# Kernel tuning notes

Hardware: AMD Instinct MI355X
Metric: run time of the kernel (lower is better)

## Reference

```python
import jax, jax.numpy as jnp
import numpy as np

D_MODEL = 1024
N_HEAD = 16
HEAD_DIM = D_MODEL // N_HEAD


def setup_inputs() -> dict:
    key = jax.random.key(0)
    k1, k2, k3 = jax.random.split(key, 3)
    B, T = 2, 2048
    x = jax.random.normal(k1, (B, T, D_MODEL), dtype=jnp.float32)
    # nn.MultiheadAttention packed in-projection: (3*D, D), xavier-like scale
    w_in = jax.random.normal(k2, (3 * D_MODEL, D_MODEL), dtype=jnp.float32) * (1.0 / np.sqrt(D_MODEL))
    b_in = jnp.zeros((3 * D_MODEL,), dtype=jnp.float32)
    w_out = jax.random.normal(k3, (D_MODEL, D_MODEL), dtype=jnp.float32) * (1.0 / np.sqrt(D_MODEL))
    b_out = jnp.zeros((D_MODEL,), dtype=jnp.float32)
    return {"x": x, "w_in": w_in, "b_in": b_in, "w_out": w_out, "b_out": b_out}


def reference(x, w_in, b_in, w_out, b_out):
    B, T, D = x.shape
    H, hd = N_HEAD, HEAD_DIM
    # packed QKV projection (torch Linear convention: y = x @ W.T + b)
    qkv = x @ w_in.T + b_in                      # [B, T, 3D]
    q, k, v = jnp.split(qkv, 3, axis=-1)
    # [B, H, T, hd]
    q = q.reshape(B, T, H, hd).transpose(0, 2, 1, 3)
    k = k.reshape(B, T, H, hd).transpose(0, 2, 1, 3)
    v = v.reshape(B, T, H, hd).transpose(0, 2, 1, 3)
    scale = 1.0 / np.sqrt(hd).astype(np.float32)
    scores = jnp.einsum("bhqd,bhkd->bhqk", q * scale, k)  # [B, H, T, T]
    causal = jnp.tril(jnp.ones((T, T), dtype=bool))
    scores = jnp.where(causal, scores, jnp.finfo(scores.dtype).min)
    attn = jax.nn.softmax(scores, axis=-1)
    ctx = jnp.einsum("bhqk,bhkd->bhqd", attn, v)           # [B, H, T, hd]
    ctx = ctx.transpose(0, 2, 1, 3).reshape(B, T, D)
    return ctx @ w_out.T + b_out
```

## Files before the change

### kernel.cpp

```cpp
#include <hip/hip_runtime.h>


#define T_SEQ 2048
#define D_MODEL 1024
#define NEG_BIG (-1.0e30f)
#define Q_SCALE 0.18033688f

typedef float f32x4 __attribute__((ext_vector_type(4)));
typedef short s16x8 __attribute__((ext_vector_type(8)));
typedef __bf16 bf16x8 __attribute__((ext_vector_type(8)));

__device__ __forceinline__ f32x4 mfma16(s16x8 a, s16x8 b, f32x4 c) {
    return __builtin_amdgcn_mfma_f32_16x16x32_bf16(
        __builtin_bit_cast(bf16x8, a), __builtin_bit_cast(bf16x8, b), c, 0, 0, 0);
}

__device__ __forceinline__ short f2bf(float f) {
    unsigned int u = __float_as_uint(f);
    u += 0x7fffu + ((u >> 16) & 1u);
    return (short)(u >> 16);
}
__device__ __forceinline__ float bf2f(short s) {
    return __uint_as_float(((unsigned int)(unsigned short)s) << 16);
}
__device__ __forceinline__ unsigned cvt_pk_bf16(float lo, float hi) {
    unsigned r;
    asm("v_cvt_pk_bf16_f32 %0, %1, %2" : "=v"(r) : "v"(lo), "v"(hi));
    return r;
}

__device__ __forceinline__ void async_lds16(const short* g, short* l) {
    __builtin_amdgcn_global_load_lds(
        (const __attribute__((address_space(1))) unsigned int*)g,
        (__attribute__((address_space(3))) unsigned int*)l, 16, 0, 0);
}

#define N_X   4194304
#define N_WI  3145728
#define N_BI  3072
#define N_WO  1048576
#define N_BO  1024
#define V_X   (N_X  / 4)
#define V_WI  (N_WI / 4)
#define V_BI  (N_BI / 4)
#define V_WO  (N_WO / 4)
#define V_BO  (N_BO / 4)
#define V_TOT (V_X + V_WI + V_BI + V_WO + V_BO)

__global__ __launch_bounds__(256) void canon_all_kernel(
    const float* __restrict__ x, const float* __restrict__ wi,
    const float* __restrict__ bi, const float* __restrict__ wo,
    const float* __restrict__ bo,
    short* __restrict__ xb, short* __restrict__ wib, short* __restrict__ bib,
    short* __restrict__ wob, short* __restrict__ bob)
{
    int i = blockIdx.x * 256 + threadIdx.x;
    if (i >= V_TOT) return;
    const float* src; short* dst; int off;
    if      (i < V_X)                    { src = x;  dst = xb;  off = i; }
    else if (i < V_X+V_WI)               { src = wi; dst = wib; off = i - V_X; }
    else if (i < V_X+V_WI+V_BI)          { src = bi; dst = bib; off = i - V_X - V_WI; }
    else if (i < V_X+V_WI+V_BI+V_WO)     { src = wo; dst = wob; off = i - V_X - V_WI - V_BI; }
    else                                 { src = bo; dst = bob; off = i - V_X - V_WI - V_BI - V_WO; }
    float4 v = ((const float4*)src)[off];
    short4 o = { f2bf(v.x), f2bf(v.y), f2bf(v.z), f2bf(v.w) };
    ((short4*)dst)[off] = o;
}

__global__ __launch_bounds__(512, 6) void gemm_qkv_kernel(
    const short* __restrict__ A, const short* __restrict__ B,
    const short* __restrict__ bias,
    short* __restrict__ qo, short* __restrict__ ko, short* __restrict__ vto)
{
    const int K = 1024;
    alignas(16) __shared__ short As[128][32];
    alignas(16) __shared__ short Bs[128][32];
    const int m0 = blockIdx.x * 128;
    const int n0 = blockIdx.y * 128;
    const int tid = threadIdx.x;
    const int lane = tid & 63;
    const int w = tid >> 6;
    const int wm = (w & 3) * 32;
    const int wn = (w >> 2) * 64;
    const int quad = lane >> 4, l16 = lane & 15;

    f32x4 acc[2][4];
    const f32x4 zero = {0.f, 0.f, 0.f, 0.f};
#pragma unroll
    for (int i = 0; i < 2; ++i)
#pragma unroll
        for (int j = 0; j < 4; ++j) acc[i][j] = zero;

    const int lrow = lane >> 2;
    const int lcol = (lane & 3) * 8;
    const short* gA = &A[(m0 + w*16 + lrow) * K + lcol];
    const short* gB = &B[(n0 + w*16 + lrow) * K + lcol];
    short* lA = &As[w*16][0];
    short* lB = &Bs[w*16][0];

    for (int k0 = 0; k0 < K; k0 += 32) {
        __syncthreads();
        async_lds16(gA + k0, lA);
        async_lds16(gB + k0, lB);
        __syncthreads();

        s16x8 af[2], bfr[4];
#pragma unroll
        for (int i = 0; i < 2; ++i) af[i]  = *(const s16x8*)&As[wm + i*16 + l16][quad*8];
#pragma unroll
        for (int j = 0; j < 4; ++j) bfr[j] = *(const s16x8*)&Bs[wn + j*16 + l16][quad*8];
#pragma unroll
        for (int i = 0; i < 2; ++i)
#pragma unroll
            for (int j = 0; j < 4; ++j)
                acc[i][j] = mfma16(af[i], bfr[j], acc[i][j]);
    }

#pragma unroll
    for (int j = 0; j < 4; ++j) {
        int n = n0 + wn + j*16 + l16;
        float bi = bf2f(bias[n]);
        int which = n >> 10;
        int h = (n >> 6) & 15, d = n & 63;
        if (which < 2) {
            short* dst = (which == 0) ? qo : ko;
            float scl = (which == 0) ? Q_SCALE : 1.0f;
#pragma unroll
            for (int i = 0; i < 2; ++i) {
#pragma unroll
                for (int r = 0; r < 4; ++r) {
                    int m = m0 + wm + i*16 + quad*4 + r;
                    int b = m >> 11, t = m & 2047;
                    float v = (acc[i][j][r] + bi) * scl;
                    dst[(((b*16 + h) * 2048) + t) * 64 + d] = f2bf(v);
                }
            }
        } else {
#pragma unroll
            for (int i = 0; i < 2; ++i) {
                int m = m0 + wm + i*16 + quad*4;
                int b = m >> 11, t0 = m & 2047;
                short4 o4 = { f2bf(acc[i][j][0] + bi), f2bf(acc[i][j][1] + bi),
                              f2bf(acc[i][j][2] + bi), f2bf(acc[i][j][3] + bi) };
                *(short4*)&vto[(((size_t)(b*16 + h) * 64) + d) * 2048 + t0] = o4;
            }
        }
    }
}

__global__ __launch_bounds__(512) void attn_kernel(
    const short* __restrict__ Q, const short* __restrict__ K,
    const short* __restrict__ Vt, short* __restrict__ ctx)
{
    alignas(16) __shared__ short Ks[64][72];
    alignas(16) __shared__ short Vs[64][72];
    alignas(16) __shared__ short Pl[8][16][72];

    const int bh = blockIdx.x;
    const int j  = blockIdx.y;
    const int tid = threadIdx.x;
    const int w = tid >> 6, lane = tid & 63;
    const int quad = lane >> 4, l16 = lane & 15;
    const int b = bh >> 4, h = bh & 15;

    const int isB = w >> 2;
    const int wq  = w & 3;
    const int qt  = isB ? (31 - j) : j;
    const int qbase  = qt * 64;
    const int qbaseA = j * 64;
    const int qbaseB = (31 - j) * 64;

    const short* Qb  = Q  + bh * T_SEQ * 64;
    const short* Kb  = K  + bh * T_SEQ * 64;
    const short* Vbt = Vt + (size_t)bh * 64 * T_SEQ;

    const int qg = qbase + wq*16 + l16;
    const short* qrow = Qb + qg * 64;
    const s16x8 qa0 = *(const s16x8*)(qrow + quad*8);
    const s16x8 qa1 = *(const s16x8*)(qrow + 32 + quad*8);

    const s16x8 ones = { (short)0x3F80, (short)0x3F80, (short)0x3F80, (short)0x3F80,
                         (short)0x3F80, (short)0x3F80, (short)0x3F80, (short)0x3F80 };

    const f32x4 zero = {0.f, 0.f, 0.f, 0.f};
    f32x4 o[4];
#pragma unroll
    for (int dt = 0; dt < 4; ++dt) o[dt] = zero;
    f32x4 ls = zero;

    const int sr  = tid >> 3;
    const int scl = (tid & 7) * 8;

    float4 kf = *(const float4*)&Kb[sr * 64 + scl];
    float4 vf = *(const float4*)&Vbt[(size_t)sr * T_SEQ + scl];

    for (int s0 = 0; s0 <= qbaseB; s0 += 64) {
        __syncthreads();
        *(float4*)&Ks[sr][scl] = kf;
        *(float4*)&Vs[sr][scl] = vf;
        __syncthreads();

        if (s0 + 64 <= qbaseB) {
            kf = *(const float4*)&Kb[(s0 + 64 + sr) * 64 + scl];
            vf = *(const float4*)&Vbt[(size_t)sr * T_SEQ + s0 + 64 + scl];
        }

        const bool act = isB || (s0 <= qbaseA);
        if (act) {
#pragma unroll
            for (int sub = 0; sub < 4; ++sub) {
                s16x8 ka0 = *(const s16x8*)&Ks[sub*16 + l16][quad*8];
                s16x8 ka1 = *(const s16x8*)&Ks[sub*16 + l16][32 + quad*8];
                __builtin_amdgcn_s_setprio(1);
                f32x4 S = mfma16(ka1, qa1, mfma16(ka0, qa0, zero));
                __builtin_amdgcn_s_setprio(0);
                if (s0 == qbase) {
                    int sb = s0 + sub*16 + quad*4;
#pragma unroll
                    for (int r = 0; r < 4; ++r)
                        if (sb + r > qg) S[r] = NEG_BIG;
                }
                float p0 = exp2f(S[0]), p1 = exp2f(S[1]);
                float p2 = exp2f(S[2]), p3 = exp2f(S[3]);
                uint2 pk;
                pk.x = cvt_pk_bf16(p0, p1);
                pk.y = cvt_pk_bf16(p2, p3);
                *(uint2*)&Pl[w][l16][sub*16 + quad*4] = pk;
            }

            s16x8 pb0 = *(const s16x8*)&Pl[w][l16][quad*8];
            s16x8 pb1 = *(const s16x8*)&Pl[w][l16][32 + quad*8];
            __builtin_amdgcn_s_setprio(1);
            ls = mfma16(ones, pb1, mfma16(ones, pb0, ls));
#pragma unroll
            for (int dt = 0; dt < 4; ++dt) {
                s16x8 va0 = *(const s16x8*)&Vs[dt*16 + l16][quad*8];
                s16x8 va1 = *(const s16x8*)&Vs[dt*16 + l16][32 + quad*8];
                o[dt] = mfma16(va1, pb1, mfma16(va0, pb0, o[dt]));
            }
            __builtin_amdgcn_s_setprio(0);
        }
    }

    float inv = 1.0f / ls[0];
    int base = (b * T_SEQ + qg) * D_MODEL + h * 64;
#pragma unroll
    for (int dt = 0; dt < 4; ++dt) {
        uint2 pk;
        pk.x = cvt_pk_bf16(o[dt][0] * inv, o[dt][1] * inv);
        pk.y = cvt_pk_bf16(o[dt][2] * inv, o[dt][3] * inv);
        *(uint2*)&ctx[base + dt*16 + quad*4] = pk;
    }
}

__global__ __launch_bounds__(512, 4) void gemm_out_kernel(
    const short* __restrict__ A, const short* __restrict__ B,
    const short* __restrict__ bias, float* __restrict__ out)
{
    const int K = 1024;
    alignas(16) __shared__ short As[128][32];
    alignas(16) __shared__ short Bs[64][32];
    const int m0 = blockIdx.x * 128;
    const int n0 = blockIdx.y * 64;
    const int tid = threadIdx.x;
    const int lane = tid & 63;
    const int w = tid >> 6;
    const int wm = (w & 3) * 32;
    const int wn = (w >> 2) * 32;
    const int quad = lane >> 4, l16 = lane & 15;

    f32x4 acc[2][2];
    const f32x4 zero = {0.f, 0.f, 0.f, 0.f};
#pragma unroll
    for (int i = 0; i < 2; ++i)
#pragma unroll
        for (int j = 0; j < 2; ++j) acc[i][j] = zero;

    const int lrow = lane >> 2;
    const int lcol = (lane & 3) * 8;
    const short* gA = &A[(m0 + w*16 + lrow) * K + lcol];
    const short* gB = &B[(n0 + (w & 3)*16 + lrow) * K + lcol];
    short* lA = &As[w*16][0];
    short* lB = &Bs[(w & 3)*16][0];
    const bool stageB = (w < 4);

    for (int k0 = 0; k0 < K; k0 += 32) {
        __syncthreads();
        async_lds16(gA + k0, lA);
        if (stageB) async_lds16(gB + k0, lB);
        __syncthreads();

        s16x8 af[2], bfr[2];
#pragma unroll
        for (int i = 0; i < 2; ++i) af[i]  = *(const s16x8*)&As[wm + i*16 + l16][quad*8];
#pragma unroll
        for (int j = 0; j < 2; ++j) bfr[j] = *(const s16x8*)&Bs[wn + j*16 + l16][quad*8];
#pragma unroll
        for (int i = 0; i < 2; ++i)
#pragma unroll
            for (int j = 0; j < 2; ++j)
                acc[i][j] = mfma16(af[i], bfr[j], acc[i][j]);
    }

#pragma unroll
    for (int j = 0; j < 2; ++j) {
        int n = n0 + wn + j*16 + l16;
        float bi = bf2f(bias[n]);
#pragma unroll
        for (int i = 0; i < 2; ++i) {
#pragma unroll
            for (int r = 0; r < 4; ++r) {
                int m = m0 + wm + i*16 + quad*4 + r;
                out[m * 1024 + n] = acc[i][j][r] + bi;
            }
        }
    }
}

extern "C" void kernel_launch(void* const* d_in, const int* in_sizes, int n_in,
                              void* d_out, int out_size, void* d_ws, size_t ws_size,
                              hipStream_t stream) {
    float* out = (float*)d_out;
    char* ws = (char*)d_ws;

    const size_t MB = 1u << 20;
    short* xb     = (short*)(ws);
    short* w_inb  = (short*)(ws + 8*MB);
    short* b_inb  = (short*)(ws + 14*MB);
    short* w_outb = (short*)(ws + 15*MB);
    short* b_outb = (short*)(ws + 17*MB);
    short* qb     = (short*)(ws + 18*MB);
    short* kb     = (short*)(ws + 26*MB);
    short* vtb    = (short*)(ws + 34*MB);
    short* ctxb   = (short*)(ws + 42*MB);

    canon_all_kernel<<<(V_TOT + 255) / 256, 256, 0, stream>>>(
        (const float*)d_in[0], (const float*)d_in[1], (const float*)d_in[2],
        (const float*)d_in[3], (const float*)d_in[4],
        xb, w_inb, b_inb, w_outb, b_outb);

    gemm_qkv_kernel<<<dim3(32, 24), 512, 0, stream>>>(xb, w_inb, b_inb, qb, kb, vtb);
    attn_kernel<<<dim3(32, 16), 512, 0, stream>>>(qb, kb, vtb, ctxb);
    gemm_out_kernel<<<dim3(32, 16), 512, 0, stream>>>(ctxb, w_outb, b_outb, out);
}
```

Measured before the change: 174.2 us.

## Split QK^T across waves by key sub-tile and share P via LDS

```diff
diff --git a/kernel.cpp b/kernel.cpp
--- a/kernel.cpp
+++ b/kernel.cpp
@@ -154,7 +154,7 @@
 {
     alignas(16) __shared__ short Ks[64][72];
     alignas(16) __shared__ short Vs[64][72];
-    alignas(16) __shared__ short Pl[8][16][72];
+    alignas(16) __shared__ short Pg[2][64][72];
 
     const int bh = blockIdx.x;
     const int j  = blockIdx.y;
@@ -174,10 +174,14 @@
     const short* Kb  = K  + bh * T_SEQ * 64;
     const short* Vbt = Vt + (size_t)bh * 64 * T_SEQ;
 
+    s16x8 qa0[4], qa1[4];
+#pragma unroll
+    for (int qq = 0; qq < 4; ++qq) {
+        const short* qrow = Qb + (qbase + qq*16 + l16) * 64;
+        qa0[qq] = *(const s16x8*)(qrow + quad*8);
+        qa1[qq] = *(const s16x8*)(qrow + 32 + quad*8);
+    }
     const int qg = qbase + wq*16 + l16;
-    const short* qrow = Qb + qg * 64;
-    const s16x8 qa0 = *(const s16x8*)(qrow + quad*8);
-    const s16x8 qa1 = *(const s16x8*)(qrow + 32 + quad*8);
 
     const s16x8 ones = { (short)0x3F80, (short)0x3F80, (short)0x3F80, (short)0x3F80,
                          (short)0x3F80, (short)0x3F80, (short)0x3F80, (short)0x3F80 };
@@ -207,29 +211,33 @@
 
         const bool act = isB || (s0 <= qbaseA);
         if (act) {
-#pragma unroll
-            for (int sub = 0; sub < 4; ++sub) {
-                s16x8 ka0 = *(const s16x8*)&Ks[sub*16 + l16][quad*8];
-                s16x8 ka1 = *(const s16x8*)&Ks[sub*16 + l16][32 + quad*8];
+            s16x8 ka0 = *(const s16x8*)&Ks[wq*16 + l16][quad*8];
+            s16x8 ka1 = *(const s16x8*)&Ks[wq*16 + l16][32 + quad*8];
+#pragma unroll
+            for (int qq = 0; qq < 4; ++qq) {
                 __builtin_amdgcn_s_setprio(1);
-                f32x4 S = mfma16(ka1, qa1, mfma16(ka0, qa0, zero));
+                f32x4 S = mfma16(ka1, qa1[qq], mfma16(ka0, qa0[qq], zero));
                 __builtin_amdgcn_s_setprio(0);
                 if (s0 == qbase) {
-                    int sb = s0 + sub*16 + quad*4;
+                    int sb = s0 + wq*16 + quad*4;
+                    int qglob = qbase + qq*16 + l16;
 #pragma unroll
                     for (int r = 0; r < 4; ++r)
-                        if (sb + r > qg) S[r] = NEG_BIG;
+                        if (sb + r > qglob) S[r] = NEG_BIG;
                 }
                 float p0 = exp2f(S[0]), p1 = exp2f(S[1]);
                 float p2 = exp2f(S[2]), p3 = exp2f(S[3]);
                 uint2 pk;
                 pk.x = cvt_pk_bf16(p0, p1);
                 pk.y = cvt_pk_bf16(p2, p3);
-                *(uint2*)&Pl[w][l16][sub*16 + quad*4] = pk;
-            }
-
-            s16x8 pb0 = *(const s16x8*)&Pl[w][l16][quad*8];
-            s16x8 pb1 = *(const s16x8*)&Pl[w][l16][32 + quad*8];
+                *(uint2*)&Pg[isB][qq*16 + l16][wq*16 + quad*4] = pk;
+            }
+        }
+        __syncthreads();
+
+        if (act) {
+            s16x8 pb0 = *(const s16x8*)&Pg[isB][wq*16 + l16][quad*8];
+            s16x8 pb1 = *(const s16x8*)&Pg[isB][wq*16 + l16][32 + quad*8];
             __builtin_amdgcn_s_setprio(1);
             ls = mfma16(ones, pb1, mfma16(ones, pb0, ls));
 #pragma unroll
```

Result: no change. 175.9 us (+1.0%).

## Drop LDS staging of K/V in attention and read tiles directly from global

Applied to the files above, without the earlier changes.

```diff
diff --git a/kernel.cpp b/kernel.cpp
--- a/kernel.cpp
+++ b/kernel.cpp
@@ -148,33 +148,25 @@
     }
 }
 
-__global__ __launch_bounds__(512) void attn_kernel(
+__global__ __launch_bounds__(256) void attn_kernel(
     const short* __restrict__ Q, const short* __restrict__ K,
     const short* __restrict__ Vt, short* __restrict__ ctx)
 {
-    alignas(16) __shared__ short Ks[64][72];
-    alignas(16) __shared__ short Vs[64][72];
-    alignas(16) __shared__ short Pl[8][16][72];
+    alignas(16) __shared__ short Pl[4][16][72];
 
     const int bh = blockIdx.x;
-    const int j  = blockIdx.y;
+    const int qt = 31 - (int)blockIdx.y;
+    const int qbase = qt * 64;
     const int tid = threadIdx.x;
     const int w = tid >> 6, lane = tid & 63;
     const int quad = lane >> 4, l16 = lane & 15;
     const int b = bh >> 4, h = bh & 15;
 
-    const int isB = w >> 2;
-    const int wq  = w & 3;
-    const int qt  = isB ? (31 - j) : j;
-    const int qbase  = qt * 64;
-    const int qbaseA = j * 64;
-    const int qbaseB = (31 - j) * 64;
-
     const short* Qb  = Q  + bh * T_SEQ * 64;
     const short* Kb  = K  + bh * T_SEQ * 64;
     const short* Vbt = Vt + (size_t)bh * 64 * T_SEQ;
 
-    const int qg = qbase + wq*16 + l16;
+    const int qg = qbase + w*16 + l16;
     const short* qrow = Qb + qg * 64;
     const s16x8 qa0 = *(const s16x8*)(qrow + quad*8);
     const s16x8 qa1 = *(const s16x8*)(qrow + 32 + quad*8);
@@ -188,58 +180,54 @@
     for (int dt = 0; dt < 4; ++dt) o[dt] = zero;
     f32x4 ls = zero;
 
-    const int sr  = tid >> 3;
-    const int scl = (tid & 7) * 8;
-
-    float4 kf = *(const float4*)&Kb[sr * 64 + scl];
-    float4 vf = *(const float4*)&Vbt[(size_t)sr * T_SEQ + scl];
-
-    for (int s0 = 0; s0 <= qbaseB; s0 += 64) {
-        __syncthreads();
-        *(float4*)&Ks[sr][scl] = kf;
-        *(float4*)&Vs[sr][scl] = vf;
-        __syncthreads();
-
-        if (s0 + 64 <= qbaseB) {
-            kf = *(const float4*)&Kb[(s0 + 64 + sr) * 64 + scl];
-            vf = *(const float4*)&Vbt[(size_t)sr * T_SEQ + s0 + 64 + scl];
+    const short* vrow0 = Vbt + (size_t)(      l16) * T_SEQ;
+    const short* vrow1 = Vbt + (size_t)(16 + l16) * T_SEQ;
+    const short* vrow2 = Vbt + (size_t)(32 + l16) * T_SEQ;
+    const short* vrow3 = Vbt + (size_t)(48 + l16) * T_SEQ;
+
+    for (int s0 = 0; s0 <= qbase; s0 += 64) {
+#pragma unroll
+        for (int sub = 0; sub < 4; ++sub) {
+            const short* krow = Kb + (s0 + sub*16 + l16) * 64;
+            s16x8 ka0 = *(const s16x8*)(krow + quad*8);
+            s16x8 ka1 = *(const s16x8*)(krow + 32 + quad*8);
+            __builtin_amdgcn_s_setprio(1);
+            f32x4 S = mfma16(ka1, qa1, mfma16(ka0, qa0, zero));
+            __builtin_amdgcn_s_setprio(0);
+            if (s0 == qbase) {
+                int sb = s0 + sub*16 + quad*4;
+#pragma unroll
+                for (int r = 0; r < 4; ++r)
+                    if (sb + r > qg) S[r] = NEG_BIG;
+            }
+            float p0 = exp2f(S[0]), p1 = exp2f(S[1]);
+            float p2 = exp2f(S[2]), p3 = exp2f(S[3]);
+            uint2 pk;
+            pk.x = cvt_pk_bf16(p0, p1);
+            pk.y = cvt_pk_bf16(p2, p3);
+            *(uint2*)&Pl[w][l16][sub*16 + quad*4] = pk;
         }
 
-        const bool act = isB || (s0 <= qbaseA);
-        if (act) {
-#pragma unroll
-            for (int sub = 0; sub < 4; ++sub) {
-                s16x8 ka0 = *(const s16x8*)&Ks[sub*16 + l16][quad*8];
-                s16x8 ka1 = *(const s16x8*)&Ks[sub*16 + l16][32 + quad*8];
-                __builtin_amdgcn_s_setprio(1);
-                f32x4 S = mfma16(ka1, qa1, mfma16(ka0, qa0, zero));
-                __builtin_amdgcn_s_setprio(0);
-                if (s0 == qbase) {
-                    int sb = s0 + sub*16 + quad*4;
-#pragma unroll
-                    for (int r = 0; r < 4; ++r)
-                        if (sb + r > qg) S[r] = NEG_BIG;
-                }
-                float p0 = exp2f(S[0]), p1 = exp2f(S[1]);
-                float p2 = exp2f(S[2]), p3 = exp2f(S[3]);
-                uint2 pk;
-                pk.x = cvt_pk_bf16(p0, p1);
-                pk.y = cvt_pk_bf16(p2, p3);
-                *(uint2*)&Pl[w][l16][sub*16 + quad*4] = pk;
-            }
-
-            s16x8 pb0 = *(const s16x8*)&Pl[w][l16][quad*8];
-            s16x8 pb1 = *(const s16x8*)&Pl[w][l16][32 + quad*8];
-            __builtin_amdgcn_s_setprio(1);
-            ls = mfma16(ones, pb1, mfma16(ones, pb0, ls));
-#pragma unroll
-            for (int dt = 0; dt < 4; ++dt) {
-                s16x8 va0 = *(const s16x8*)&Vs[dt*16 + l16][quad*8];
-                s16x8 va1 = *(const s16x8*)&Vs[dt*16 + l16][32 + quad*8];
-                o[dt] = mfma16(va1, pb1, mfma16(va0, pb0, o[dt]));
-            }
-            __builtin_amdgcn_s_setprio(0);
+        s16x8 pb0 = *(const s16x8*)&Pl[w][l16][quad*8];
+        s16x8 pb1 = *(const s16x8*)&Pl[w][l16][32 + quad*8];
+        __builtin_amdgcn_s_setprio(1);
+        ls = mfma16(ones, pb1, mfma16(ones, pb0, ls));
+        {
+            s16x8 va0, va1;
+            va0 = *(const s16x8*)(vrow0 + s0 + quad*8);
+            va1 = *(const s16x8*)(vrow0 + s0 + 32 + quad*8);
+            o[0] = mfma16(va1, pb1, mfma16(va0, pb0, o[0]));
+            va0 = *(const s16x8*)(vrow1 + s0 + quad*8);
+            va1 = *(const s16x8*)(vrow1 + s0 + 32 + quad*8);
+            o[1] = mfma16(va1, pb1, mfma16(va0, pb0, o[1]));
+            va0 = *(const s16x8*)(vrow2 + s0 + quad*8);
+            va1 = *(const s16x8*)(vrow2 + s0 + 32 + quad*8);
+            o[2] = mfma16(va1, pb1, mfma16(va0, pb0, o[2]));
+            va0 = *(const s16x8*)(vrow3 + s0 + quad*8);
+            va1 = *(const s16x8*)(vrow3 + s0 + 32 + quad*8);
+            o[3] = mfma16(va1, pb1, mfma16(va0, pb0, o[3]));
         }
+        __builtin_amdgcn_s_setprio(0);
     }
 
     float inv = 1.0f / ls[0];
@@ -340,6 +328,6 @@
         xb, w_inb, b_inb, w_outb, b_outb);
 
     gemm_qkv_kernel<<<dim3(32, 24), 512, 0, stream>>>(xb, w_inb, b_inb, qb, kb, vtb);
-    attn_kernel<<<dim3(32, 16), 512, 0, stream>>>(qb, kb, vtb, ctxb);
+    attn_kernel<<<dim3(32, 32), 256, 0, stream>>>(qb, kb, vtb, ctxb);
     gemm_out_kernel<<<dim3(32, 16), 512, 0, stream>>>(ctxb, w_outb, b_outb, out);
 }
```

After: 279.3 us. +60.3%, slower.

## Split attention KV range across two wave groups per query tile with LDS reduction

Applied to the files above, without the earlier changes.

```diff
diff --git a/kernel.cpp b/kernel.cpp
--- a/kernel.cpp
+++ b/kernel.cpp
@@ -152,23 +152,24 @@
     const short* __restrict__ Q, const short* __restrict__ K,
     const short* __restrict__ Vt, short* __restrict__ ctx)
 {
-    alignas(16) __shared__ short Ks[64][72];
-    alignas(16) __shared__ short Vs[64][72];
+    alignas(16) __shared__ short Ks[2][64][72];
+    alignas(16) __shared__ short Vs[2][64][72];
     alignas(16) __shared__ short Pl[8][16][72];
 
     const int bh = blockIdx.x;
-    const int j  = blockIdx.y;
+    const int qt = 31 - (int)blockIdx.y;
+    const int qbase = qt * 64;
     const int tid = threadIdx.x;
     const int w = tid >> 6, lane = tid & 63;
     const int quad = lane >> 4, l16 = lane & 15;
     const int b = bh >> 4, h = bh & 15;
 
-    const int isB = w >> 2;
-    const int wq  = w & 3;
-    const int qt  = isB ? (31 - j) : j;
-    const int qbase  = qt * 64;
-    const int qbaseA = j * 64;
-    const int qbaseB = (31 - j) * 64;
+    const int g  = w >> 2;
+    const int wq = w & 3;
+    const int h0 = (qt + 2) >> 1;
+    const int h1 = (qt + 1) >> 1;
+    const int myN   = g ? h1 : h0;
+    const int sbase = g ? h0 : 0;
 
     const short* Qb  = Q  + bh * T_SEQ * 64;
     const short* Kb  = K  + bh * T_SEQ * 64;
@@ -188,37 +189,51 @@
     for (int dt = 0; dt < 4; ++dt) o[dt] = zero;
     f32x4 ls = zero;
 
-    const int sr  = tid >> 3;
-    const int scl = (tid & 7) * 8;
-
-    float4 kf = *(const float4*)&Kb[sr * 64 + scl];
-    float4 vf = *(const float4*)&Vbt[(size_t)sr * T_SEQ + scl];
-
-    for (int s0 = 0; s0 <= qbaseB; s0 += 64) {
-        __syncthreads();
-        *(float4*)&Ks[sr][scl] = kf;
-        *(float4*)&Vs[sr][scl] = vf;
-        __syncthreads();
-
-        if (s0 + 64 <= qbaseB) {
-            kf = *(const float4*)&Kb[(s0 + 64 + sr) * 64 + scl];
-            vf = *(const float4*)&Vbt[(size_t)sr * T_SEQ + s0 + 64 + scl];
-        }
-
-        const bool act = isB || (s0 <= qbaseA);
-        if (act) {
+    const int t8 = tid & 255;
+    const int sr = t8 >> 2;
+    const int sc = (t8 & 3) * 16;
+
+    float4 kf0, kf1, vf0, vf1;
+    {
+        int s0 = sbase * 64;
+        kf0 = *(const float4*)&Kb[(s0 + sr) * 64 + sc];
+        kf1 = *(const float4*)&Kb[(s0 + sr) * 64 + sc + 8];
+        vf0 = *(const float4*)&Vbt[(size_t)sr * T_SEQ + s0 + sc];
+        vf1 = *(const float4*)&Vbt[(size_t)sr * T_SEQ + s0 + sc + 8];
+    }
+
+    for (int r = 0; r < h0; ++r) {
+        __syncthreads();
+        if (r < myN) {
+            *(float4*)&Ks[g][sr][sc]     = kf0;
+            *(float4*)&Ks[g][sr][sc + 8] = kf1;
+            *(float4*)&Vs[g][sr][sc]     = vf0;
+            *(float4*)&Vs[g][sr][sc + 8] = vf1;
+        }
+        __syncthreads();
+
+        if (r + 1 < myN) {
+            int s0 = (sbase + r + 1) * 64;
+            kf0 = *(const float4*)&Kb[(s0 + sr) * 64 + sc];
+            kf1 = *(const float4*)&Kb[(s0 + sr) * 64 + sc + 8];
+            vf0 = *(const float4*)&Vbt[(size_t)sr * T_SEQ + s0 + sc];
+            vf1 = *(const float4*)&Vbt[(size_t)sr * T_SEQ + s0 + sc + 8];
+        }
+
+        if (r < myN) {
+            const int s0 = (sbase + r) * 64;
 #pragma unroll
             for (int sub = 0; sub < 4; ++sub) {
-                s16x8 ka0 = *(const s16x8*)&Ks[sub*16 + l16][quad*8];
-                s16x8 ka1 = *(const s16x8*)&Ks[sub*16 + l16][32 + quad*8];
+                s16x8 ka0 = *(const s16x8*)&Ks[g][sub*16 + l16][quad*8];
+                s16x8 ka1 = *(const s16x8*)&Ks[g][sub*16 + l16][32 + quad*8];
                 __builtin_amdgcn_s_setprio(1);
                 f32x4 S = mfma16(ka1, qa1, mfma16(ka0, qa0, zero));
                 __builtin_amdgcn_s_setprio(0);
                 if (s0 == qbase) {
                     int sb = s0 + sub*16 + quad*4;
 #pragma unroll
-                    for (int r = 0; r < 4; ++r)
-                        if (sb + r > qg) S[r] = NEG_BIG;
+                    for (int rr = 0; rr < 4; ++rr)
+                        if (sb + rr > qg) S[rr] = NEG_BIG;
                 }
                 float p0 = exp2f(S[0]), p1 = exp2f(S[1]);
                 float p2 = exp2f(S[2]), p3 = exp2f(S[3]);
@@ -234,22 +249,42 @@
             ls = mfma16(ones, pb1, mfma16(ones, pb0, ls));
 #pragma unroll
             for (int dt = 0; dt < 4; ++dt) {
-                s16x8 va0 = *(const s16x8*)&Vs[dt*16 + l16][quad*8];
-                s16x8 va1 = *(const s16x8*)&Vs[dt*16 + l16][32 + quad*8];
+                s16x8 va0 = *(const s16x8*)&Vs[g][dt*16 + l16][quad*8];
+                s16x8 va1 = *(const s16x8*)&Vs[g][dt*16 + l16][32 + quad*8];
                 o[dt] = mfma16(va1, pb1, mfma16(va0, pb0, o[dt]));
             }
             __builtin_amdgcn_s_setprio(0);
         }
     }
 
-    float inv = 1.0f / ls[0];
-    int base = (b * T_SEQ + qg) * D_MODEL + h * 64;
-#pragma unroll
-    for (int dt = 0; dt < 4; ++dt) {
-        uint2 pk;
-        pk.x = cvt_pk_bf16(o[dt][0] * inv, o[dt][1] * inv);
-        pk.y = cvt_pk_bf16(o[dt][2] * inv, o[dt][3] * inv);
-        *(uint2*)&ctx[base + dt*16 + quad*4] = pk;
+    __syncthreads();
+    float* cb = (float*)&Pl[0][0][0];
+    if (g) {
+        float* p = cb + t8 * 17;
+#pragma unroll
+        for (int dt = 0; dt < 4; ++dt) {
+            p[dt*4 + 0] = o[dt][0]; p[dt*4 + 1] = o[dt][1];
+            p[dt*4 + 2] = o[dt][2]; p[dt*4 + 3] = o[dt][3];
+        }
+        p[16] = ls[0];
+    }
+    __syncthreads();
+    if (!g) {
+        const float* p = cb + tid * 17;
+#pragma unroll
+        for (int dt = 0; dt < 4; ++dt) {
+            o[dt][0] += p[dt*4 + 0]; o[dt][1] += p[dt*4 + 1];
+            o[dt][2] += p[dt*4 + 2]; o[dt][3] += p[dt*4 + 3];
+        }
+        float inv = 1.0f / (ls[0] + p[16]);
+        int base = (b * T_SEQ + qg) * D_MODEL + h * 64;
+#pragma unroll
+        for (int dt = 0; dt < 4; ++dt) {
+            uint2 pk;
+            pk.x = cvt_pk_bf16(o[dt][0] * inv, o[dt][1] * inv);
+            pk.y = cvt_pk_bf16(o[dt][2] * inv, o[dt][3] * inv);
+            *(uint2*)&ctx[base + dt*16 + quad*4] = pk;
+        }
     }
 }
 
@@ -340,6 +375,6 @@
         xb, w_inb, b_inb, w_outb, b_outb);
 
     gemm_qkv_kernel<<<dim3(32, 24), 512, 0, stream>>>(xb, w_inb, b_inb, qb, kb, vtb);
-    attn_kernel<<<dim3(32, 16), 512, 0, stream>>>(qb, kb, vtb, ctxb);
+    attn_kernel<<<dim3(32, 32), 512, 0, stream>>>(qb, kb, vtb, ctxb);
     gemm_out_kernel<<<dim3(32, 16), 512, 0, stream>>>(ctxb, w_outb, b_outb, out);
 }
```

New measurement: 174.3 us. Within noise of the previous version (+0.1%).
